# Kernel tuning notes

Hardware: AMD Instinct MI355X
Metric: run time of the kernel (lower is better)

## Reference

```python
import jax, jax.numpy as jnp
import numpy as np

HIDDEN = 1024
N_HEAD = 16
HEAD_DIM = HIDDEN // N_HEAD


def setup_inputs() -> dict:
    key = jax.random.key(0)
    k1, k2, k3 = jax.random.split(key, 3)
    B, S = 4, 2048
    x = jax.random.normal(k1, (B, S, HIDDEN), dtype=jnp.float32)
    # nn.Linear(hidden, 3*hidden, bias=False): weight [3*hidden, hidden]
    w_qkv = jax.random.normal(k2, (3 * HIDDEN, HIDDEN), dtype=jnp.float32) * (HIDDEN ** -0.5)
    w_out = jax.random.normal(k3, (HIDDEN, HIDDEN), dtype=jnp.float32) * (HIDDEN ** -0.5)
    return {"x": x, "w_qkv": w_qkv, "w_out": w_out}


def _rope(q, k):
    # q, k: [B, H, S, D]
    S, D = q.shape[-2], q.shape[-1]
    pos = jnp.arange(S, dtype=jnp.float32)[:, None]          # [S, 1]
    ids = jnp.arange(D // 2, dtype=jnp.float32)              # [D/2]
    theta = jnp.power(jnp.float32(10000.0), 2.0 * ids / D)   # [D/2]
    ang = pos / theta                                        # [S, D/2]
    # torch code: sin at even slots, cos at odd slots; then repeat_interleave(2)
    sin = jnp.repeat(jnp.sin(ang), 2, axis=-1)               # [S, D]
    cos = jnp.repeat(jnp.cos(ang), 2, axis=-1)               # [S, D]

    def rot(t):
        # stack([-t_odd, t_even], -1).reshape -> interleaved rotate-half
        t2 = jnp.stack([-t[..., 1::2], t[..., 0::2]], axis=-1).reshape(t.shape)
        return t * cos + t2 * sin

    return rot(q), rot(k)


def reference(x, w_qkv, w_out):
    B, S, _ = x.shape
    qkv = jnp.einsum('bsd,ed->bse', x, w_qkv)                # [B, S, 3*hidden]
    qkv = qkv.reshape(B, S, N_HEAD, 3 * HEAD_DIM).transpose(0, 2, 1, 3)  # [B,H,S,3D]
    q, k, v = jnp.split(qkv, 3, axis=-1)                     # each [B,H,S,D]
    q, k = _rope(q, k)
    # NOTE: original forward never applies self.scale, mask (eval), or dropout.
    scores = jnp.einsum('bhqd,bhkd->bhqk', q, k)             # [B,H,S,S]
    probs = jax.nn.softmax(scores, axis=-1)
    out = jnp.einsum('bhqk,bhkd->bhqd', probs, v)            # [B,H,S,D]
    out = out.transpose(0, 2, 1, 3).reshape(B, S, HIDDEN)
    return jnp.einsum('bsd,ed->bse', out, w_out)
```

## Files before the change

### kernel.cpp

```cpp
#include <hip/hip_runtime.h>
#include <stdint.h>
#include <math.h>

#define NHEAD 16
#define HDIM 64
#define BATCH 4
#define SEQ 2048
#define NROWS (BATCH*SEQ)
#define LOG2E 1.4426950408889634f

typedef _Float16 f16x8 __attribute__((ext_vector_type(8)));
typedef _Float16 f16x4 __attribute__((ext_vector_type(4)));
typedef __fp16 h16x2 __attribute__((ext_vector_type(2)));
typedef float f32x4 __attribute__((ext_vector_type(4)));
typedef float f32x16 __attribute__((ext_vector_type(16)));
typedef unsigned int u32x4 __attribute__((ext_vector_type(4)));

typedef const __attribute__((address_space(1))) unsigned int* gas_ptr;
typedef __attribute__((address_space(3))) unsigned int* las_ptr;

__device__ __forceinline__ void gload_lds16(const void* g, void* l) {
  __builtin_amdgcn_global_load_lds((gas_ptr)g, (las_ptr)l, 16, 0, 0);
}

__device__ __forceinline__ float exp2_fast(float x) {
  float r; asm("v_exp_f32 %0, %1" : "=v"(r) : "v"(x)); return r;
}

__device__ __forceinline__ unsigned pku(float a, float b) {
  h16x2 p = __builtin_amdgcn_cvt_pkrtz(a, b);
  return __builtin_bit_cast(unsigned, p);
}

__global__ void cvt_f16_kernel(const float* __restrict__ in,
                               unsigned short* __restrict__ out, int n4) {
  int stride = gridDim.x * blockDim.x;
  for (int i = blockIdx.x * blockDim.x + threadIdx.x; i < n4; i += stride) {
    float4 v = ((const float4*)in)[i];
    f16x4 h;
    h[0] = (_Float16)v.x; h[1] = (_Float16)v.y;
    h[2] = (_Float16)v.z; h[3] = (_Float16)v.w;
    ((f16x4*)out)[i] = h;
  }
}

__global__ void sincos_kernel(float2* __restrict__ tab) {
  int idx = blockIdx.x * blockDim.x + threadIdx.x;
  int s = idx >> 5, i = idx & 31;
  float theta = powf(10000.0f, (float)i / 32.0f);
  float ang = (float)s / theta;
  tab[idx] = make_float2(sinf(ang), cosf(ang));
}

__global__ __launch_bounds__(256)
void gemm_qkv_f16(const unsigned short* __restrict__ A,
                  const unsigned short* __restrict__ B,
                  const float2* __restrict__ tab,
                  unsigned short* __restrict__ Qh,
                  unsigned short* __restrict__ Kh,
                  unsigned short* __restrict__ Vt) {
  const int K = 1024, nk = K >> 6;
  __shared__ unsigned short sA[2][128 * 64];
  __shared__ unsigned short sB[2][128 * 64];
  const int tid = threadIdx.x;
  const int lane = tid & 63;
  const int wave = tid >> 6;
  const int wr = wave >> 1, wc = wave & 1;
  const long m0 = (long)blockIdx.x * 128;
  const long n0 = (long)blockIdx.y * 128;

  f32x4 acc[4][4] = {};

  auto stage = [&](int buf, int kt) {
    const long k0 = (long)kt * 64;
    const char* Ab = (const char*)A;
    const char* Bb = (const char*)B;
#pragma unroll
    for (int qd = 0; qd < 4; ++qd) {
      int o = qd * 4096 + tid * 16;
      int row = o >> 7;
      int colb = (((o >> 4) & 7) ^ (row & 7)) << 4;
      gload_lds16(Ab + ((m0 + row) * K + k0) * 2 + colb, (char*)&sA[buf][0] + o);
      gload_lds16(Bb + ((n0 + row) * K + k0) * 2 + colb, (char*)&sB[buf][0] + o);
    }
  };

  const int lhi = lane >> 4, llo = lane & 15;
  const int rA = wr * 64 + llo;
  const int rB = wc * 64 + llo;
  int chsw[2];
#pragma unroll
  for (int s = 0; s < 2; ++s) chsw[s] = (((s * 4 + lhi) ^ (llo & 7)) << 3);

  stage(0, 0);
  __syncthreads();
  int cur = 0;

  for (int kt = 0; kt < nk; ++kt) {
    if (kt + 1 < nk) stage(cur ^ 1, kt + 1);
    f16x8 af[2][4], bfr[2][4];
#pragma unroll
    for (int s = 0; s < 2; ++s)
#pragma unroll
      for (int m = 0; m < 4; ++m)
        af[s][m] = *(const f16x8*)&sA[cur][(rA + m * 16) * 64 + chsw[s]];
#pragma unroll
    for (int s = 0; s < 2; ++s)
#pragma unroll
      for (int n = 0; n < 4; ++n)
        bfr[s][n] = *(const f16x8*)&sB[cur][(rB + n * 16) * 64 + chsw[s]];
#pragma unroll
    for (int m = 0; m < 4; ++m)
#pragma unroll
      for (int n = 0; n < 4; ++n) {
        acc[m][n] = __builtin_amdgcn_mfma_f32_16x16x32_f16(af[0][m], bfr[0][n], acc[m][n], 0, 0, 0);
        acc[m][n] = __builtin_amdgcn_mfma_f32_16x16x32_f16(af[1][m], bfr[1][n], acc[m][n], 0, 0, 0);
      }
    __syncthreads();
    cur ^= 1;
  }

  const int rb0 = (int)m0 + wr * 64 + lhi * 4;
  const int bidx = rb0 >> 11;
  const int s0 = rb0 & 2047;
#pragma unroll
  for (int n = 0; n < 4; ++n) {
    const int col = (int)n0 + wc * 64 + llo + n * 16;
    const int h = col / 192;
    const int off = col - h * 192;
    const int part = off >> 6;
    const int d = off & 63;
    const long bh_ = (long)(bidx * 16 + h);
    if (part < 2) {
      _Float16* dst = (_Float16*)(part == 0 ? Qh : Kh) + bh_ * SEQ * 64 + d;
      const float qs = (part == 0) ? LOG2E : 1.0f;
      const float2* tp = tab + (d >> 1);
      const int sgn = d & 1;
#pragma unroll
      for (int m = 0; m < 4; ++m)
#pragma unroll
        for (int r = 0; r < 4; ++r) {
          int s = s0 + m * 16 + r;
          float v = acc[m][n][r];
          float p = __shfl_xor(v, 1, 64);
          float2 sc = tp[s * 32];
          float rot = sgn ? (v * sc.y + p * sc.x) : (v * sc.y - p * sc.x);
          dst[(long)s * 64] = (_Float16)(rot * qs);
        }
    } else {
      _Float16* dst = (_Float16*)Vt + (bh_ * 64 + d) * SEQ;
#pragma unroll
      for (int m = 0; m < 4; ++m)
#pragma unroll
        for (int r = 0; r < 4; ++r)
          dst[s0 + m * 16 + r] = (_Float16)acc[m][n][r];
    }
  }
}

__global__ __launch_bounds__(512, 3)
void attn_kernel(const unsigned short* __restrict__ Qh,
                 const unsigned short* __restrict__ Kh,
                 const unsigned short* __restrict__ Vt,
                 unsigned short* __restrict__ AOut) {
  __shared__ unsigned short sK[2][64 * 64];
  __shared__ unsigned short sV[2][64 * 64];

  const int tid = threadIdx.x;
  const int w = tid >> 6, lane = tid & 63;
  const int q32 = lane & 31, hi = lane >> 5;
  const int bh = blockIdx.y, b = bh >> 4, h = bh & 15;
  const int q = blockIdx.x * 256 + w * 32 + q32;

  f16x8 aq[4];
#pragma unroll
  for (int ds = 0; ds < 4; ++ds)
    aq[ds] = *(const f16x8*)&Qh[((long)bh * SEQ + q) * 64 + ds * 16 + hi * 8];

  f32x16 acc0 = {}, acc1 = {};
  float mrow = -INFINITY, lrow = 0.f;

  const int r7 = q32 & 7;
  int off[2][4];
#pragma unroll
  for (int t = 0; t < 2; ++t)
#pragma unroll
    for (int s = 0; s < 4; ++s)
      off[t][s] = (t * 32 + q32) * 64 + (((s * 2 + hi) ^ r7) << 3);

  const int cr = tid >> 3, cp = tid & 7, cps = cp ^ (cr & 7);
  const long kSrc0 = ((long)bh * SEQ + cr) * 64 + cps * 8;
  const long vSrc0 = ((long)bh * 64 + cr) * SEQ + cps * 8;

  auto stage = [&](int buf, int kt) {
    gload_lds16(&Kh[kSrc0 + (long)kt * 4096], (char*)&sK[buf][0] + tid * 16);
    gload_lds16(&Vt[vSrc0 + (long)kt * 64],   (char*)&sV[buf][0] + tid * 16);
  };

  stage(0, 0);
  __syncthreads();

#define MKPA(dst, S, R0) {                                        \
    unsigned A0 = pku(S[R0 + 0], S[R0 + 1]);                      \
    unsigned A1 = pku(S[R0 + 2], S[R0 + 3]);                      \
    unsigned B0 = pku(S[R0 + 4], S[R0 + 5]);                      \
    unsigned B1 = pku(S[R0 + 6], S[R0 + 7]);                      \
    asm("v_permlane32_swap_b32 %0, %1" : "+v"(A0), "+v"(B0));     \
    asm("v_permlane32_swap_b32 %0, %1" : "+v"(A1), "+v"(B1));     \
    u32x4 tt; tt[0] = A0; tt[1] = A1; tt[2] = B0; tt[3] = B1;     \
    dst = __builtin_bit_cast(f16x8, tt); }

#pragma unroll 2
  for (int kt = 0; kt < SEQ / 64; ++kt) {
    const int cur = kt & 1;
    if (kt + 1 < SEQ / 64) stage(cur ^ 1, kt + 1);
    const unsigned short* Kb = &sK[cur][0];
    const unsigned short* Vb = &sV[cur][0];

    f32x16 s0v = {}, s1v = {};
    __builtin_amdgcn_s_setprio(1);
#pragma unroll
    for (int ds = 0; ds < 4; ++ds) {
      f16x8 k0 = *(const f16x8*)&Kb[off[0][ds]];
      f16x8 k1 = *(const f16x8*)&Kb[off[1][ds]];
      s0v = __builtin_amdgcn_mfma_f32_32x32x16_f16(k0, aq[ds], s0v, 0, 0, 0);
      s1v = __builtin_amdgcn_mfma_f32_32x32x16_f16(k1, aq[ds], s1v, 0, 0, 0);
    }
    __builtin_amdgcn_s_setprio(0);

    float ta[16];
#pragma unroll
    for (int r = 0; r < 16; ++r) ta[r] = fmaxf(s0v[r], s1v[r]);
#pragma unroll
    for (int d = 8; d > 0; d >>= 1)
#pragma unroll
      for (int r = 0; r < d; ++r) ta[r] = fmaxf(ta[r], ta[r + d]);
    float tmax = fmaxf(ta[0], __shfl_xor(ta[0], 32, 64));

    if (__any(tmax > mrow + 8.0f)) {
      float mnew = fmaxf(mrow, tmax);
      float al = exp2_fast(mrow - mnew);
      mrow = mnew;
#pragma unroll
      for (int r = 0; r < 16; ++r) { acc0[r] *= al; acc1[r] *= al; }
      lrow *= al;
    }
    const float mr = mrow;

#pragma unroll
    for (int r = 0; r < 16; ++r) {
      s0v[r] = exp2_fast(s0v[r] - mr);
      s1v[r] = exp2_fast(s1v[r] - mr);
    }

    float sa[16];
#pragma unroll
    for (int r = 0; r < 16; ++r) sa[r] = s0v[r] + s1v[r];
#pragma unroll
    for (int d = 8; d > 0; d >>= 1)
#pragma unroll
      for (int r = 0; r < d; ++r) sa[r] = sa[r] + sa[r + d];
    lrow += sa[0] + __shfl_xor(sa[0], 32, 64);

    f16x8 pa[4];
    MKPA(pa[0], s0v, 0);
    MKPA(pa[1], s0v, 8);
    MKPA(pa[2], s1v, 0);
    MKPA(pa[3], s1v, 8);

    __builtin_amdgcn_s_setprio(1);
#pragma unroll
    for (int ks = 0; ks < 4; ++ks) {
      f16x8 v0 = *(const f16x8*)&Vb[off[0][ks]];
      f16x8 v1 = *(const f16x8*)&Vb[off[1][ks]];
      acc0 = __builtin_amdgcn_mfma_f32_32x32x16_f16(v0, pa[ks], acc0, 0, 0, 0);
      acc1 = __builtin_amdgcn_mfma_f32_32x32x16_f16(v1, pa[ks], acc1, 0, 0, 0);
    }
    __builtin_amdgcn_s_setprio(0);
    __syncthreads();
  }

  float inv = 1.f / lrow;
  const long obase = ((long)b * SEQ + q) * 1024 + h * 64;
#define EPI(ACCV, DT)                                              \
  {                                                                \
    _Pragma("unroll")                                              \
    for (int rg = 0; rg < 4; ++rg) {                               \
      f16x4 o;                                                     \
      _Pragma("unroll")                                            \
      for (int e = 0; e < 4; ++e)                                  \
        o[e] = (_Float16)(ACCV[rg * 4 + e] * inv);                 \
      *(f16x4*)&AOut[obase + DT * 32 + rg * 8 + hi * 4] = o;       \
    }                                                              \
  }
  EPI(acc0, 0);
  EPI(acc1, 1);
}

__global__ __launch_bounds__(256)
void gemm_out_f16(const unsigned short* __restrict__ A,
                  const unsigned short* __restrict__ B,
                  float* __restrict__ C, int M, int N, int K) {
  __shared__ unsigned short sA[2][128 * 64];
  __shared__ unsigned short sB[2][128 * 64];
  const int tid = threadIdx.x;
  const int lane = tid & 63;
  const int wave = tid >> 6;
  const int wr = wave >> 1, wc = wave & 1;
  const long m0 = (long)blockIdx.x * 128;
  const long n0 = (long)blockIdx.y * 128;

  f32x4 acc[4][4] = {};

  auto stage = [&](int buf, int kt) {
    const long k0 = (long)kt * 64;
    const char* Ab = (const char*)A;
    const char* Bb = (const char*)B;
#pragma unroll
    for (int qd = 0; qd < 4; ++qd) {
      int o = qd * 4096 + tid * 16;
      int row = o >> 7;
      int colb = (((o >> 4) & 7) ^ (row & 7)) << 4;
      gload_lds16(Ab + ((m0 + row) * K + k0) * 2 + colb, (char*)&sA[buf][0] + o);
      gload_lds16(Bb + ((n0 + row) * K + k0) * 2 + colb, (char*)&sB[buf][0] + o);
    }
  };

  const int lhi = lane >> 4, llo = lane & 15;
  const int rA = wr * 64 + llo;
  const int rB = wc * 64 + llo;
  int chsw[2];
#pragma unroll
  for (int s = 0; s < 2; ++s) chsw[s] = (((s * 4 + lhi) ^ (llo & 7)) << 3);

  const int nk = K >> 6;
  stage(0, 0);
  __syncthreads();
  int cur = 0;

  for (int kt = 0; kt < nk; ++kt) {
    if (kt + 1 < nk) stage(cur ^ 1, kt + 1);
    f16x8 af[2][4], bfr[2][4];
#pragma unroll
    for (int s = 0; s < 2; ++s)
#pragma unroll
      for (int m = 0; m < 4; ++m)
        af[s][m] = *(const f16x8*)&sA[cur][(rA + m * 16) * 64 + chsw[s]];
#pragma unroll
    for (int s = 0; s < 2; ++s)
#pragma unroll
      for (int n = 0; n < 4; ++n)
        bfr[s][n] = *(const f16x8*)&sB[cur][(rB + n * 16) * 64 + chsw[s]];
#pragma unroll
    for (int m = 0; m < 4; ++m)
#pragma unroll
      for (int n = 0; n < 4; ++n) {
        acc[m][n] = __builtin_amdgcn_mfma_f32_16x16x32_f16(af[0][m], bfr[0][n], acc[m][n], 0, 0, 0);
        acc[m][n] = __builtin_amdgcn_mfma_f32_16x16x32_f16(af[1][m], bfr[1][n], acc[m][n], 0, 0, 0);
      }
    __syncthreads();
    cur ^= 1;
  }

  const long rbase = m0 + wr * 64 + lhi * 4;
#pragma unroll
  for (int n = 0; n < 4; ++n) {
    const long col = n0 + wc * 64 + llo + n * 16;
#pragma unroll
    for (int m = 0; m < 4; ++m)
#pragma unroll
      for (int r = 0; r < 4; ++r)
        C[(rbase + m * 16 + r) * N + col] = acc[m][n][r];
  }
}

extern "C" void kernel_launch(void* const* d_in, const int* in_sizes, int n_in,
                              void* d_out, int out_size, void* d_ws, size_t ws_size,
                              hipStream_t stream) {
  const float* x     = (const float*)d_in[0];
  const float* w_qkv = (const float*)d_in[1];
  const float* w_out = (const float*)d_in[2];
  float* out = (float*)d_out;
  char* ws = (char*)d_ws;

  unsigned short* xb    = (unsigned short*)(ws + 0);
  unsigned short* attnb = xb;
  unsigned short* wqkvb = (unsigned short*)(ws + 16777216);
  unsigned short* woutb = (unsigned short*)(ws + 23068672);
  unsigned short* Qh    = (unsigned short*)(ws + 25165824);
  unsigned short* Kh    = (unsigned short*)(ws + 41943040);
  unsigned short* Vt    = (unsigned short*)(ws + 58720256);
  float2*         tab   = (float2*)(ws + 75497472);

  cvt_f16_kernel<<<2048, 256, 0, stream>>>(x, xb, NROWS * 1024 / 4);
  cvt_f16_kernel<<<1024, 256, 0, stream>>>(w_qkv, wqkvb, 3072 * 1024 / 4);
  cvt_f16_kernel<<<512, 256, 0, stream>>>(w_out, woutb, 1024 * 1024 / 4);
  sincos_kernel<<<SEQ * 32 / 256, 256, 0, stream>>>(tab);

  gemm_qkv_f16<<<dim3(64, 24), 256, 0, stream>>>(xb, wqkvb, tab, Qh, Kh, Vt);
  attn_kernel<<<dim3(SEQ / 256, 64), 512, 0, stream>>>(Qh, Kh, Vt, attnb);
  gemm_out_f16<<<dim3(64, 8), 256, 0, stream>>>(attnb, woutb, out, NROWS, 1024, 1024);
}
```

Measured before the change: 213.1 us.

## Software-pipeline attention with 4-stage LDS ring and MFMA row-sum

Restructures the attention kernel into a software pipeline: the QK^T MFMAs for tile t+1 are issued before the softmax and PV of tile t, and K/V are prefetched three tiles ahead into a 4-deep LDS ring using explicit vmcnt waits instead of __syncthreads. The softmax row sum is moved onto the matrix unit by multiplying P with a ones vector, which removes the shuffle/add reduction. Block size drops from 512 to 256 threads (128 queries per block, twice as many blocks). The changes aim to hide LDS/global latency and the softmax VALU work behind MFMA, at the cost of more registers and LDS per block, extra MFMA work for the sum, and lower occupancy.

```diff
diff --git a/kernel.cpp b/kernel.cpp
--- a/kernel.cpp
+++ b/kernel.cpp
@@ -158,27 +158,28 @@
   }
 }
 
-__global__ __launch_bounds__(512, 3)
+__global__ __launch_bounds__(256, 2)
 void attn_kernel(const unsigned short* __restrict__ Qh,
                  const unsigned short* __restrict__ Kh,
                  const unsigned short* __restrict__ Vt,
                  unsigned short* __restrict__ AOut) {
-  __shared__ unsigned short sK[2][64 * 64];
-  __shared__ unsigned short sV[2][64 * 64];
-
+  __shared__ unsigned short sK[4][64 * 64];
+  __shared__ unsigned short sV[4][64 * 64];
+
+  const int NT = SEQ / 64;
   const int tid = threadIdx.x;
   const int w = tid >> 6, lane = tid & 63;
   const int q32 = lane & 31, hi = lane >> 5;
   const int bh = blockIdx.y, b = bh >> 4, h = bh & 15;
-  const int q = blockIdx.x * 256 + w * 32 + q32;
+  const int q = blockIdx.x * 128 + w * 32 + q32;
 
   f16x8 aq[4];
 #pragma unroll
   for (int ds = 0; ds < 4; ++ds)
     aq[ds] = *(const f16x8*)&Qh[((long)bh * SEQ + q) * 64 + ds * 16 + hi * 8];
 
-  f32x16 acc0 = {}, acc1 = {};
-  float mrow = -INFINITY, lrow = 0.f;
+  f32x16 acc0 = {}, acc1 = {}, accl = {};
+  float mrow = -INFINITY;
 
   const int r7 = q32 & 7;
   int off[2][4];
@@ -188,17 +189,22 @@
     for (int s = 0; s < 4; ++s)
       off[t][s] = (t * 32 + q32) * 64 + (((s * 2 + hi) ^ r7) << 3);
 
-  const int cr = tid >> 3, cp = tid & 7, cps = cp ^ (cr & 7);
-  const long kSrc0 = ((long)bh * SEQ + cr) * 64 + cps * 8;
-  const long vSrc0 = ((long)bh * 64 + cr) * SEQ + cps * 8;
+  const int r0s = tid >> 3, cp = tid & 7, cps = cp ^ (r0s & 7);
+  const long kA0 = ((long)bh * SEQ + r0s) * 64 + cps * 8;
+  const long vA0 = ((long)bh * 64 + r0s) * SEQ + cps * 8;
 
   auto stage = [&](int buf, int kt) {
-    gload_lds16(&Kh[kSrc0 + (long)kt * 4096], (char*)&sK[buf][0] + tid * 16);
-    gload_lds16(&Vt[vSrc0 + (long)kt * 64],   (char*)&sV[buf][0] + tid * 16);
+    char* kd = (char*)&sK[buf][0] + tid * 16;
+    char* vd = (char*)&sV[buf][0] + tid * 16;
+    gload_lds16(&Kh[kA0 + (long)kt * 4096], kd);
+    gload_lds16(&Kh[kA0 + 2048 + (long)kt * 4096], kd + 4096);
+    gload_lds16(&Vt[vA0 + (long)kt * 64], vd);
+    gload_lds16(&Vt[vA0 + 32 * SEQ + (long)kt * 64], vd + 4096);
   };
 
-  stage(0, 0);
-  __syncthreads();
+  f16x8 vones;
+#pragma unroll
+  for (int j = 0; j < 8; ++j) vones[j] = (_Float16)1.0f;
 
 #define MKPA(dst, S, R0) {                                        \
     unsigned A0 = pku(S[R0 + 0], S[R0 + 1]);                      \
@@ -210,27 +216,25 @@
     u32x4 tt; tt[0] = A0; tt[1] = A1; tt[2] = B0; tt[3] = B1;     \
     dst = __builtin_bit_cast(f16x8, tt); }
 
-#pragma unroll 2
-  for (int kt = 0; kt < SEQ / 64; ++kt) {
-    const int cur = kt & 1;
-    if (kt + 1 < SEQ / 64) stage(cur ^ 1, kt + 1);
-    const unsigned short* Kb = &sK[cur][0];
-    const unsigned short* Vb = &sV[cur][0];
-
-    f32x16 s0v = {}, s1v = {};
+  auto qk = [&](int t1, f32x16& n0, f32x16& n1) {
+    const unsigned short* Kb = &sK[t1 & 3][0];
+    f32x16 z0 = {}, z1 = {};
     __builtin_amdgcn_s_setprio(1);
 #pragma unroll
     for (int ds = 0; ds < 4; ++ds) {
       f16x8 k0 = *(const f16x8*)&Kb[off[0][ds]];
       f16x8 k1 = *(const f16x8*)&Kb[off[1][ds]];
-      s0v = __builtin_amdgcn_mfma_f32_32x32x16_f16(k0, aq[ds], s0v, 0, 0, 0);
-      s1v = __builtin_amdgcn_mfma_f32_32x32x16_f16(k1, aq[ds], s1v, 0, 0, 0);
+      z0 = __builtin_amdgcn_mfma_f32_32x32x16_f16(k0, aq[ds], z0, 0, 0, 0);
+      z1 = __builtin_amdgcn_mfma_f32_32x32x16_f16(k1, aq[ds], z1, 0, 0, 0);
     }
     __builtin_amdgcn_s_setprio(0);
-
+    n0 = z0; n1 = z1;
+  };
+
+  auto smpv = [&](int t, f32x16& c0, f32x16& c1) {
     float ta[16];
 #pragma unroll
-    for (int r = 0; r < 16; ++r) ta[r] = fmaxf(s0v[r], s1v[r]);
+    for (int r = 0; r < 16; ++r) ta[r] = fmaxf(c0[r], c1[r]);
 #pragma unroll
     for (int d = 8; d > 0; d >>= 1)
 #pragma unroll
@@ -242,32 +246,23 @@
       float al = exp2_fast(mrow - mnew);
       mrow = mnew;
 #pragma unroll
-      for (int r = 0; r < 16; ++r) { acc0[r] *= al; acc1[r] *= al; }
-      lrow *= al;
+      for (int r = 0; r < 16; ++r) { acc0[r] *= al; acc1[r] *= al; accl[r] *= al; }
     }
     const float mr = mrow;
 
 #pragma unroll
     for (int r = 0; r < 16; ++r) {
-      s0v[r] = exp2_fast(s0v[r] - mr);
-      s1v[r] = exp2_fast(s1v[r] - mr);
-    }
-
-    float sa[16];
-#pragma unroll
-    for (int r = 0; r < 16; ++r) sa[r] = s0v[r] + s1v[r];
-#pragma unroll
-    for (int d = 8; d > 0; d >>= 1)
-#pragma unroll
-      for (int r = 0; r < d; ++r) sa[r] = sa[r] + sa[r + d];
-    lrow += sa[0] + __shfl_xor(sa[0], 32, 64);
+      c0[r] = exp2_fast(c0[r] - mr);
+      c1[r] = exp2_fast(c1[r] - mr);
+    }
 
     f16x8 pa[4];
-    MKPA(pa[0], s0v, 0);
-    MKPA(pa[1], s0v, 8);
-    MKPA(pa[2], s1v, 0);
-    MKPA(pa[3], s1v, 8);
-
+    MKPA(pa[0], c0, 0);
+    MKPA(pa[1], c0, 8);
+    MKPA(pa[2], c1, 0);
+    MKPA(pa[3], c1, 8);
+
+    const unsigned short* Vb = &sV[t & 3][0];
     __builtin_amdgcn_s_setprio(1);
 #pragma unroll
     for (int ks = 0; ks < 4; ++ks) {
@@ -275,12 +270,36 @@
       f16x8 v1 = *(const f16x8*)&Vb[off[1][ks]];
       acc0 = __builtin_amdgcn_mfma_f32_32x32x16_f16(v0, pa[ks], acc0, 0, 0, 0);
       acc1 = __builtin_amdgcn_mfma_f32_32x32x16_f16(v1, pa[ks], acc1, 0, 0, 0);
+      accl = __builtin_amdgcn_mfma_f32_32x32x16_f16(vones, pa[ks], accl, 0, 0, 0);
     }
     __builtin_amdgcn_s_setprio(0);
-    __syncthreads();
-  }
-
-  float inv = 1.f / lrow;
+  };
+
+#define ITER(T, C0, C1, N0, N1)                                   \
+  {                                                               \
+    if ((T) + 3 < NT) stage(((T) + 3) & 3, (T) + 3);              \
+    qk((T) + 1, N0, N1);                                          \
+    smpv((T), C0, C1);                                            \
+    if ((T) + 3 < NT) asm volatile("s_waitcnt vmcnt(4)");         \
+    else              asm volatile("s_waitcnt vmcnt(0)");         \
+    __builtin_amdgcn_s_barrier();                                 \
+  }
+
+  stage(0, 0); stage(1, 1); stage(2, 2);
+  asm volatile("s_waitcnt vmcnt(4)");
+  __builtin_amdgcn_s_barrier();
+
+  f32x16 sA0, sA1, sB0, sB1;
+  qk(0, sA0, sA1);
+
+  for (int t2 = 0; t2 < NT - 2; t2 += 2) {
+    ITER(t2,     sA0, sA1, sB0, sB1);
+    ITER(t2 + 1, sB0, sB1, sA0, sA1);
+  }
+  ITER(NT - 2, sA0, sA1, sB0, sB1);
+  smpv(NT - 1, sB0, sB1);
+
+  float inv = 1.f / accl[0];
   const long obase = ((long)b * SEQ + q) * 1024 + h * 64;
 #define EPI(ACCV, DT)                                              \
   {                                                                \
@@ -398,6 +417,6 @@
   sincos_kernel<<<SEQ * 32 / 256, 256, 0, stream>>>(tab);
 
   gemm_qkv_f16<<<dim3(64, 24), 256, 0, stream>>>(xb, wqkvb, tab, Qh, Kh, Vt);
-  attn_kernel<<<dim3(SEQ / 256, 64), 512, 0, stream>>>(Qh, Kh, Vt, attnb);
+  attn_kernel<<<dim3(SEQ / 128, 64), 256, 0, stream>>>(Qh, Kh, Vt, attnb);
   gemm_out_f16<<<dim3(64, 8), 256, 0, stream>>>(attnb, woutb, out, NROWS, 1024, 1024);
 }
```

New measurement: 228.1 us. 1.07x slower.

## Shrink attention blocks, remap grid per XCD, compute row sums via MFMA

Applied to the files above, without the earlier changes.

The attention kernel now runs 256-thread blocks covering 128 queries, launched as a flat 1024-block grid. Block ids are remapped so blocks of the same batch-head land on the same XCD, which is meant to improve K/V cache reuse. Each thread now issues two K and two V async loads per tile to fill the shared buffers. The row-sum reduction is replaced by an extra MFMA against a vector of ones, and the max reduction uses v_max3. This trades extra matrix work and accumulator registers for fewer VALU and shuffle ops, with more blocks and more frequent block-level syncs.

```diff
diff --git a/kernel.cpp b/kernel.cpp
--- a/kernel.cpp
+++ b/kernel.cpp
@@ -25,6 +25,10 @@
 
 __device__ __forceinline__ float exp2_fast(float x) {
   float r; asm("v_exp_f32 %0, %1" : "=v"(r) : "v"(x)); return r;
+}
+
+__device__ __forceinline__ float max3f(float a, float b, float c) {
+  float r; asm("v_max3_f32 %0, %1, %2, %3" : "=v"(r) : "v"(a), "v"(b), "v"(c)); return r;
 }
 
 __device__ __forceinline__ unsigned pku(float a, float b) {
@@ -158,7 +162,7 @@
   }
 }
 
-__global__ __launch_bounds__(512, 3)
+__global__ __launch_bounds__(256, 3)
 void attn_kernel(const unsigned short* __restrict__ Qh,
                  const unsigned short* __restrict__ Kh,
                  const unsigned short* __restrict__ Vt,
@@ -166,19 +170,25 @@
   __shared__ unsigned short sK[2][64 * 64];
   __shared__ unsigned short sV[2][64 * 64];
 
+  const int NT = SEQ / 64;
   const int tid = threadIdx.x;
   const int w = tid >> 6, lane = tid & 63;
   const int q32 = lane & 31, hi = lane >> 5;
-  const int bh = blockIdx.y, b = bh >> 4, h = bh & 15;
-  const int q = blockIdx.x * 256 + w * 32 + q32;
+
+  const int bid = blockIdx.x;
+  const int xcd = bid & 7, rest = bid >> 3;
+  const int bh = (rest >> 4) * 8 + xcd;
+  const int qt = rest & 15;
+  const int b = bh >> 4, h = bh & 15;
+  const int q = qt * 128 + w * 32 + q32;
 
   f16x8 aq[4];
 #pragma unroll
   for (int ds = 0; ds < 4; ++ds)
     aq[ds] = *(const f16x8*)&Qh[((long)bh * SEQ + q) * 64 + ds * 16 + hi * 8];
 
-  f32x16 acc0 = {}, acc1 = {};
-  float mrow = -INFINITY, lrow = 0.f;
+  f32x16 acc0 = {}, acc1 = {}, accl = {};
+  float mrow = -INFINITY;
 
   const int r7 = q32 & 7;
   int off[2][4];
@@ -188,17 +198,22 @@
     for (int s = 0; s < 4; ++s)
       off[t][s] = (t * 32 + q32) * 64 + (((s * 2 + hi) ^ r7) << 3);
 
-  const int cr = tid >> 3, cp = tid & 7, cps = cp ^ (cr & 7);
-  const long kSrc0 = ((long)bh * SEQ + cr) * 64 + cps * 8;
-  const long vSrc0 = ((long)bh * 64 + cr) * SEQ + cps * 8;
+  const int r0s = tid >> 3, cp = tid & 7, cps = cp ^ (r0s & 7);
+  const long kA0 = ((long)bh * SEQ + r0s) * 64 + cps * 8;
+  const long vA0 = ((long)bh * 64 + r0s) * SEQ + cps * 8;
 
   auto stage = [&](int buf, int kt) {
-    gload_lds16(&Kh[kSrc0 + (long)kt * 4096], (char*)&sK[buf][0] + tid * 16);
-    gload_lds16(&Vt[vSrc0 + (long)kt * 64],   (char*)&sV[buf][0] + tid * 16);
+    char* kd = (char*)&sK[buf][0] + tid * 16;
+    char* vd = (char*)&sV[buf][0] + tid * 16;
+    gload_lds16(&Kh[kA0 + (long)kt * 4096], kd);
+    gload_lds16(&Kh[kA0 + 2048 + (long)kt * 4096], kd + 4096);
+    gload_lds16(&Vt[vA0 + (long)kt * 64], vd);
+    gload_lds16(&Vt[vA0 + 32 * SEQ + (long)kt * 64], vd + 4096);
   };
 
-  stage(0, 0);
-  __syncthreads();
+  f16x8 vones;
+#pragma unroll
+  for (int j = 0; j < 8; ++j) vones[j] = (_Float16)1.0f;
 
 #define MKPA(dst, S, R0) {                                        \
     unsigned A0 = pku(S[R0 + 0], S[R0 + 1]);                      \
@@ -210,10 +225,13 @@
     u32x4 tt; tt[0] = A0; tt[1] = A1; tt[2] = B0; tt[3] = B1;     \
     dst = __builtin_bit_cast(f16x8, tt); }
 
+  stage(0, 0);
+  __syncthreads();
+
 #pragma unroll 2
-  for (int kt = 0; kt < SEQ / 64; ++kt) {
+  for (int kt = 0; kt < NT; ++kt) {
     const int cur = kt & 1;
-    if (kt + 1 < SEQ / 64) stage(cur ^ 1, kt + 1);
+    if (kt + 1 < NT) stage(cur ^ 1, kt + 1);
     const unsigned short* Kb = &sK[cur][0];
     const unsigned short* Vb = &sV[cur][0];
 
@@ -228,22 +246,30 @@
     }
     __builtin_amdgcn_s_setprio(0);
 
-    float ta[16];
-#pragma unroll
-    for (int r = 0; r < 16; ++r) ta[r] = fmaxf(s0v[r], s1v[r]);
-#pragma unroll
-    for (int d = 8; d > 0; d >>= 1)
-#pragma unroll
-      for (int r = 0; r < d; ++r) ta[r] = fmaxf(ta[r], ta[r + d]);
-    float tmax = fmaxf(ta[0], __shfl_xor(ta[0], 32, 64));
+    float t0 = max3f(s0v[0], s0v[1], s0v[2]);
+    float t1 = max3f(s0v[3], s0v[4], s0v[5]);
+    float t2 = max3f(s0v[6], s0v[7], s0v[8]);
+    float t3 = max3f(s0v[9], s0v[10], s0v[11]);
+    float t4 = max3f(s0v[12], s0v[13], s0v[14]);
+    float t5 = max3f(s0v[15], s1v[0], s1v[1]);
+    float t6 = max3f(s1v[2], s1v[3], s1v[4]);
+    float t7 = max3f(s1v[5], s1v[6], s1v[7]);
+    float t8 = max3f(s1v[8], s1v[9], s1v[10]);
+    float t9 = max3f(s1v[11], s1v[12], s1v[13]);
+    float t10 = fmaxf(s1v[14], s1v[15]);
+    float u0 = max3f(t0, t1, t2);
+    float u1 = max3f(t3, t4, t5);
+    float u2 = max3f(t6, t7, t8);
+    float u3 = fmaxf(t9, t10);
+    float tmax = fmaxf(max3f(u0, u1, u2), u3);
+    tmax = fmaxf(tmax, __shfl_xor(tmax, 32, 64));
 
     if (__any(tmax > mrow + 8.0f)) {
       float mnew = fmaxf(mrow, tmax);
       float al = exp2_fast(mrow - mnew);
       mrow = mnew;
 #pragma unroll
-      for (int r = 0; r < 16; ++r) { acc0[r] *= al; acc1[r] *= al; }
-      lrow *= al;
+      for (int r = 0; r < 16; ++r) { acc0[r] *= al; acc1[r] *= al; accl[r] *= al; }
     }
     const float mr = mrow;
 
@@ -252,15 +278,6 @@
       s0v[r] = exp2_fast(s0v[r] - mr);
       s1v[r] = exp2_fast(s1v[r] - mr);
     }
-
-    float sa[16];
-#pragma unroll
-    for (int r = 0; r < 16; ++r) sa[r] = s0v[r] + s1v[r];
-#pragma unroll
-    for (int d = 8; d > 0; d >>= 1)
-#pragma unroll
-      for (int r = 0; r < d; ++r) sa[r] = sa[r] + sa[r + d];
-    lrow += sa[0] + __shfl_xor(sa[0], 32, 64);
 
     f16x8 pa[4];
     MKPA(pa[0], s0v, 0);
@@ -275,12 +292,13 @@
       f16x8 v1 = *(const f16x8*)&Vb[off[1][ks]];
       acc0 = __builtin_amdgcn_mfma_f32_32x32x16_f16(v0, pa[ks], acc0, 0, 0, 0);
       acc1 = __builtin_amdgcn_mfma_f32_32x32x16_f16(v1, pa[ks], acc1, 0, 0, 0);
+      accl = __builtin_amdgcn_mfma_f32_32x32x16_f16(vones, pa[ks], accl, 0, 0, 0);
     }
     __builtin_amdgcn_s_setprio(0);
     __syncthreads();
   }
 
-  float inv = 1.f / lrow;
+  float inv = 1.f / accl[0];
   const long obase = ((long)b * SEQ + q) * 1024 + h * 64;
 #define EPI(ACCV, DT)                                              \
   {                                                                \
@@ -398,6 +416,6 @@
   sincos_kernel<<<SEQ * 32 / 256, 256, 0, stream>>>(tab);
 
   gemm_qkv_f16<<<dim3(64, 24), 256, 0, stream>>>(xb, wqkvb, tab, Qh, Kh, Vt);
-  attn_kernel<<<dim3(SEQ / 256, 64), 512, 0, stream>>>(Qh, Kh, Vt, attnb);
+  attn_kernel<<<1024, 256, 0, stream>>>(Qh, Kh, Vt, attnb);
   gemm_out_f16<<<dim3(64, 8), 256, 0, stream>>>(attnb, woutb, out, NROWS, 1024, 1024);
 }
```

After: 214.1 us. Within noise of the previous version (+0.5%).

## Quad-buffer attention K/V tiles, remap blocks per XCD, use max3 reductions

Applied to the files above, without the earlier changes.

The attention kernel now keeps four LDS buffers for K and V, stages two tiles ahead, and processes two tiles between each barrier, which halves the number of __syncthreads. The grid is flattened to 1D and block IDs are remapped so that blocks of the same (batch, head) land on the same XCD, aimed at better L2 reuse of K/V. The row-max reduction uses v_max3_f32, and launch bounds are raised to 4 blocks per CU. The trade-off is doubled LDS use, 64 KB per block, and more register pressure from the higher occupancy target, which could cause spills.

```diff
diff --git a/kernel.cpp b/kernel.cpp
--- a/kernel.cpp
+++ b/kernel.cpp
@@ -25,6 +25,10 @@
 
 __device__ __forceinline__ float exp2_fast(float x) {
   float r; asm("v_exp_f32 %0, %1" : "=v"(r) : "v"(x)); return r;
+}
+
+__device__ __forceinline__ float max3f(float a, float b, float c) {
+  float r; asm("v_max3_f32 %0, %1, %2, %3" : "=v"(r) : "v"(a), "v"(b), "v"(c)); return r;
 }
 
 __device__ __forceinline__ unsigned pku(float a, float b) {
@@ -158,19 +162,25 @@
   }
 }
 
-__global__ __launch_bounds__(512, 3)
+__global__ __launch_bounds__(512, 4)
 void attn_kernel(const unsigned short* __restrict__ Qh,
                  const unsigned short* __restrict__ Kh,
                  const unsigned short* __restrict__ Vt,
                  unsigned short* __restrict__ AOut) {
-  __shared__ unsigned short sK[2][64 * 64];
-  __shared__ unsigned short sV[2][64 * 64];
-
+  __shared__ unsigned short sK[4][64 * 64];
+  __shared__ unsigned short sV[4][64 * 64];
+
+  const int NT = SEQ / 64;
   const int tid = threadIdx.x;
   const int w = tid >> 6, lane = tid & 63;
   const int q32 = lane & 31, hi = lane >> 5;
-  const int bh = blockIdx.y, b = bh >> 4, h = bh & 15;
-  const int q = blockIdx.x * 256 + w * 32 + q32;
+
+  const int bid = blockIdx.x;
+  const int xcd = bid & 7, rest = bid >> 3;
+  const int bh = (rest >> 3) * 8 + xcd;
+  const int qt = rest & 7;
+  const int b = bh >> 4, h = bh & 15;
+  const int q = qt * 256 + w * 32 + q32;
 
   f16x8 aq[4];
 #pragma unroll
@@ -196,9 +206,6 @@
     gload_lds16(&Kh[kSrc0 + (long)kt * 4096], (char*)&sK[buf][0] + tid * 16);
     gload_lds16(&Vt[vSrc0 + (long)kt * 64],   (char*)&sV[buf][0] + tid * 16);
   };
-
-  stage(0, 0);
-  __syncthreads();
 
 #define MKPA(dst, S, R0) {                                        \
     unsigned A0 = pku(S[R0 + 0], S[R0 + 1]);                      \
@@ -210,12 +217,9 @@
     u32x4 tt; tt[0] = A0; tt[1] = A1; tt[2] = B0; tt[3] = B1;     \
     dst = __builtin_bit_cast(f16x8, tt); }
 
-#pragma unroll 2
-  for (int kt = 0; kt < SEQ / 64; ++kt) {
-    const int cur = kt & 1;
-    if (kt + 1 < SEQ / 64) stage(cur ^ 1, kt + 1);
-    const unsigned short* Kb = &sK[cur][0];
-    const unsigned short* Vb = &sV[cur][0];
+  auto tile = [&](int t) {
+    const unsigned short* Kb = &sK[t & 3][0];
+    const unsigned short* Vb = &sV[t & 3][0];
 
     f32x16 s0v = {}, s1v = {};
     __builtin_amdgcn_s_setprio(1);
@@ -228,14 +232,23 @@
     }
     __builtin_amdgcn_s_setprio(0);
 
-    float ta[16];
-#pragma unroll
-    for (int r = 0; r < 16; ++r) ta[r] = fmaxf(s0v[r], s1v[r]);
-#pragma unroll
-    for (int d = 8; d > 0; d >>= 1)
-#pragma unroll
-      for (int r = 0; r < d; ++r) ta[r] = fmaxf(ta[r], ta[r + d]);
-    float tmax = fmaxf(ta[0], __shfl_xor(ta[0], 32, 64));
+    float t0 = max3f(s0v[0], s0v[1], s0v[2]);
+    float t1 = max3f(s0v[3], s0v[4], s0v[5]);
+    float t2 = max3f(s0v[6], s0v[7], s0v[8]);
+    float t3 = max3f(s0v[9], s0v[10], s0v[11]);
+    float t4 = max3f(s0v[12], s0v[13], s0v[14]);
+    float t5 = max3f(s0v[15], s1v[0], s1v[1]);
+    float t6 = max3f(s1v[2], s1v[3], s1v[4]);
+    float t7 = max3f(s1v[5], s1v[6], s1v[7]);
+    float t8 = max3f(s1v[8], s1v[9], s1v[10]);
+    float t9 = max3f(s1v[11], s1v[12], s1v[13]);
+    float t10 = fmaxf(s1v[14], s1v[15]);
+    float u0 = max3f(t0, t1, t2);
+    float u1 = max3f(t3, t4, t5);
+    float u2 = max3f(t6, t7, t8);
+    float u3 = fmaxf(t9, t10);
+    float tmax = fmaxf(max3f(u0, u1, u2), u3);
+    tmax = fmaxf(tmax, __shfl_xor(tmax, 32, 64));
 
     if (__any(tmax > mrow + 8.0f)) {
       float mnew = fmaxf(mrow, tmax);
@@ -277,6 +290,16 @@
       acc1 = __builtin_amdgcn_mfma_f32_32x32x16_f16(v1, pa[ks], acc1, 0, 0, 0);
     }
     __builtin_amdgcn_s_setprio(0);
+  };
+
+  stage(0, 0); stage(1, 1);
+  __syncthreads();
+
+  for (int it = 0; it < NT / 2; ++it) {
+    const int t0 = it * 2;
+    if (it + 1 < NT / 2) { stage((t0 + 2) & 3, t0 + 2); stage((t0 + 3) & 3, t0 + 3); }
+    tile(t0);
+    tile(t0 + 1);
     __syncthreads();
   }
 
@@ -398,6 +421,6 @@
   sincos_kernel<<<SEQ * 32 / 256, 256, 0, stream>>>(tab);
 
   gemm_qkv_f16<<<dim3(64, 24), 256, 0, stream>>>(xb, wqkvb, tab, Qh, Kh, Vt);
-  attn_kernel<<<dim3(SEQ / 256, 64), 512, 0, stream>>>(Qh, Kh, Vt, attnb);
+  attn_kernel<<<512, 512, 0, stream>>>(Qh, Kh, Vt, attnb);
   gemm_out_f16<<<dim3(64, 8), 256, 0, stream>>>(attnb, woutb, out, NROWS, 1024, 1024);
 }
```

Result: faster. 205.1 us (-3.7%).
